# Optimization experiments

Hardware: AMD Instinct MI355X
Metric: run time of the kernel (lower is better)

## Reference

```python
import jax, jax.numpy as jnp
import numpy as np

INPUT_DIM, LATENT_DIM, HIDDEN_DIM, BATCH = 1024, 128, 1024, 32768


def setup_inputs() -> dict:
    key = jax.random.key(0)
    ks = jax.random.split(key, 12)
    s = 0.02
    x = (jax.random.uniform(ks[0], (BATCH, INPUT_DIM)) < 0.5).astype(jnp.float32)  # binary data
    eps = jax.random.normal(ks[1], (BATCH, LATENT_DIM), dtype=jnp.float32)
    return {
        "x": x,
        "eps": eps,
        "We1": jax.random.normal(ks[2], (INPUT_DIM, HIDDEN_DIM)) * s,
        "be1": jnp.zeros((HIDDEN_DIM,), jnp.float32),
        "Wmu": jax.random.normal(ks[3], (HIDDEN_DIM, LATENT_DIM)) * s,
        "bmu": jnp.zeros((LATENT_DIM,), jnp.float32),
        "Wls": jax.random.normal(ks[4], (HIDDEN_DIM, LATENT_DIM)) * s,
        "bls": jnp.zeros((LATENT_DIM,), jnp.float32),
        "Wd1": jax.random.normal(ks[5], (LATENT_DIM, HIDDEN_DIM)) * s,
        "bd1": jnp.zeros((HIDDEN_DIM,), jnp.float32),
        "Wd2": jax.random.normal(ks[6], (HIDDEN_DIM, INPUT_DIM)) * s,
        "bd2": jnp.zeros((INPUT_DIM,), jnp.float32),
    }


def reference(x, eps, We1, be1, Wmu, bmu, Wls, bls, Wd1, bd1, Wd2, bd2):
    # Encoder: one hidden ReLU layer, mu / logsigma heads
    h = jax.nn.relu(x @ We1 + be1)                      # [B, H]
    mu = h @ Wmu + bmu                                  # [B, L]
    logsigma = h @ Wls + bls                            # [B, L]
    # Reparameterization: z = sigma * eps + mu (vectorized diag(exp(logsigma)) @ eps)
    z = mu + jnp.exp(logsigma) * eps                    # [B, L]
    # Decoder: one hidden ReLU layer, sigmoid Bernoulli params
    hd = jax.nn.relu(z @ Wd1 + bd1)                     # [B, H]
    theta = jax.nn.sigmoid(hd @ Wd2 + bd2)              # [B, D]
    # Bernoulli log-likelihood: sum_j log(theta^x * (1-theta)^(1-x))
    log_px = jnp.sum(x * jnp.log(theta) + (1.0 - x) * jnp.log1p(-theta), axis=-1)  # [B]
    # KL(q||N(0,I)) = 0.5 * sum(sigma^2 + mu^2 - log(sigma^2) - 1)
    kl = 0.5 * jnp.sum(jnp.exp(2.0 * logsigma) + mu * mu - 2.0 * logsigma - 1.0, axis=-1)  # [B]
    return log_px - kl                                  # elbo_mc [B]
```

## Files before the change

kernel.cpp:

```cpp
#include <hip/hip_runtime.h>
#include <cstdint>
#include <cstddef>


typedef __bf16 bf16x8 __attribute__((ext_vector_type(8)));
typedef float f32x4 __attribute__((ext_vector_type(4)));

__device__ __forceinline__ unsigned short f32_to_bf16(float f) {
  unsigned int u = __float_as_uint(f);
  u += 0x7fffu + ((u >> 16) & 1u);
  return (unsigned short)(u >> 16);
}

__global__ void cast_bf16_k(const float* __restrict__ in,
                            unsigned short* __restrict__ out, int n4) {
  int stride = gridDim.x * blockDim.x;
  for (int i = blockIdx.x * blockDim.x + threadIdx.x; i < n4; i += stride) {
    float4 v = reinterpret_cast<const float4*>(in)[i];
    ushort4 o = make_ushort4(f32_to_bf16(v.x), f32_to_bf16(v.y),
                             f32_to_bf16(v.z), f32_to_bf16(v.w));
    reinterpret_cast<ushort4*>(out)[i] = o;
  }
}

struct TransJob { const float* in; unsigned short* out; int K, N, blkEnd; };

__global__ void transpose_all_k(TransJob j0, TransJob j1, TransJob j2,
                                TransJob j3, TransJob j4) {
  __shared__ float tile[32][33];
  int bid = blockIdx.x;
  TransJob j; int base;
  if (bid < j0.blkEnd)      { j = j0; base = 0; }
  else if (bid < j1.blkEnd) { j = j1; base = j0.blkEnd; }
  else if (bid < j2.blkEnd) { j = j2; base = j1.blkEnd; }
  else if (bid < j3.blkEnd) { j = j3; base = j2.blkEnd; }
  else                      { j = j4; base = j3.blkEnd; }
  int local = bid - base;
  int gxN = j.N >> 5;
  int n0 = (local % gxN) * 32, k0 = (local / gxN) * 32;
  int tx = threadIdx.x, ty = threadIdx.y;
#pragma unroll
  for (int r = 0; r < 32; r += 8)
    tile[ty + r][tx] = j.in[(size_t)(k0 + ty + r) * j.N + n0 + tx];
  __syncthreads();
#pragma unroll
  for (int r = 0; r < 32; r += 8)
    j.out[(size_t)(n0 + ty + r) * j.K + k0 + tx] = f32_to_bf16(tile[tx][ty + r]);
}

__device__ __forceinline__ void gl_lds16(const unsigned short* g, unsigned short* l) {
  __builtin_amdgcn_global_load_lds(
      (__attribute__((address_space(1))) void*)g,
      (__attribute__((address_space(3))) void*)l, 16, 0, 0);
}

template <int EPI>
__global__ __launch_bounds__(256) void gemm_bt(
    const unsigned short* __restrict__ A, const unsigned short* __restrict__ BT,
    int gx, int N, int K,
    const float* __restrict__ bias0,
    unsigned short* __restrict__ outb, float* __restrict__ outf,
    const unsigned short* __restrict__ xbf) {
  __shared__ __align__(16) unsigned short As[128 * 64];
  __shared__ __align__(16) unsigned short Bs[128 * 64];

  const int tid = threadIdx.x;
  const int lane = tid & 63;
  const int wave = tid >> 6;
  const int wr = wave >> 1, wc = wave & 1;
  const int bid = blockIdx.x;
  const int xcd = bid & 7;
  const int t8 = bid >> 3;
  const int m0 = (xcd + 8 * (t8 / gx)) * 128;
  const int n0 = (t8 % gx) * 128;
  const int lm = lane & 15, lq = lane >> 4;

  const unsigned short* agp[4];
  const unsigned short* bgp[4];
#pragma unroll
  for (int r = 0; r < 4; ++r) {
    int c = tid + 256 * r;
    int row = c >> 3, q = (c & 7) ^ (row & 7);
    agp[r] = A + (size_t)(m0 + row) * K + q * 8;
    bgp[r] = BT + (size_t)(n0 + row) * K + q * 8;
  }
  const int sw = lm & 7;

  f32x4 acc[4][4] = {};

  for (int kt = 0; kt < K; kt += 64) {
#pragma unroll
    for (int r = 0; r < 4; ++r) {
      gl_lds16(agp[r] + kt, As + (tid + 256 * r) * 8);
      gl_lds16(bgp[r] + kt, Bs + (tid + 256 * r) * 8);
    }
    __syncthreads();

#pragma unroll
    for (int s = 0; s < 2; ++s) {
      const int so = ((s << 2) | lq) ^ sw;
      bf16x8 af[4], bfr[4];
#pragma unroll
      for (int i = 0; i < 4; ++i)
        af[i] = *reinterpret_cast<const bf16x8*>(As + (wr * 64 + i * 16 + lm) * 64 + so * 8);
#pragma unroll
      for (int j = 0; j < 4; ++j)
        bfr[j] = *reinterpret_cast<const bf16x8*>(Bs + (wc * 64 + j * 16 + lm) * 64 + so * 8);
#pragma unroll
      for (int i = 0; i < 4; ++i)
#pragma unroll
        for (int j = 0; j < 4; ++j)
          acc[i][j] = __builtin_amdgcn_mfma_f32_16x16x32_bf16(af[i], bfr[j], acc[i][j], 0, 0, 0);
    }
    __syncthreads();
  }

  if (EPI == 0) {
#pragma unroll
    for (int i = 0; i < 4; ++i)
#pragma unroll
      for (int j = 0; j < 4; ++j) {
        int col = n0 + wc * 64 + j * 16 + lm;
        float bias = bias0[col];
#pragma unroll
        for (int r = 0; r < 4; ++r) {
          int row = m0 + wr * 64 + i * 16 + lq * 4 + r;
          float v = acc[i][j][r] + bias;
          v = fmaxf(v, 0.f);
          outb[(size_t)row * N + col] = f32_to_bf16(v);
        }
      }
  } else {
#pragma unroll
    for (int i = 0; i < 4; ++i) {
      float rs[4] = {0.f, 0.f, 0.f, 0.f};
#pragma unroll
      for (int j = 0; j < 4; ++j) {
        int col = n0 + wc * 64 + j * 16 + lm;
        float bias = bias0[col];
#pragma unroll
        for (int r = 0; r < 4; ++r) {
          int row = m0 + wr * 64 + i * 16 + lq * 4 + r;
          float l = acc[i][j][r] + bias;
          unsigned short xb = xbf[(size_t)row * N + col];
          float t = xb ? -l : l;
          float sp = fmaxf(t, 0.f) + __logf(1.f + __expf(-fabsf(t)));
          rs[r] -= sp;
        }
      }
#pragma unroll
      for (int off = 1; off < 16; off <<= 1)
#pragma unroll
        for (int r = 0; r < 4; ++r) rs[r] += __shfl_xor(rs[r], off, 64);
      if (lm == 0) {
#pragma unroll
        for (int r = 0; r < 4; ++r)
          atomicAdd(&outf[m0 + wr * 64 + i * 16 + lq * 4 + r], rs[r]);
      }
    }
  }
}

__global__ __launch_bounds__(256, 1) void gemm2_zkl(
    const unsigned short* __restrict__ A,
    const unsigned short* __restrict__ BT,
    int K,
    const float* __restrict__ bmu, const float* __restrict__ bls,
    const float* __restrict__ eps,
    unsigned short* __restrict__ z,
    float* __restrict__ out) {
  __shared__ __align__(16) unsigned short As[128 * 64];
  __shared__ __align__(16) unsigned short Bs[256 * 64];

  const int tid = threadIdx.x;
  const int lane = tid & 63;
  const int wave = tid >> 6;
  const int m0 = blockIdx.x * 128;
  const int lm = lane & 15, lq = lane >> 4;

  const unsigned short* agp[4];
  const unsigned short* bgp[8];
#pragma unroll
  for (int r = 0; r < 4; ++r) {
    int c = tid + 256 * r;
    int row = c >> 3, q = (c & 7) ^ (row & 7);
    agp[r] = A + (size_t)(m0 + row) * K + q * 8;
  }
#pragma unroll
  for (int r = 0; r < 8; ++r) {
    int c = tid + 256 * r;
    int row = c >> 3, q = (c & 7) ^ (row & 7);
    bgp[r] = BT + (size_t)row * K + q * 8;
  }
  const int sw = lm & 7;

  f32x4 acc[2][16] = {};

  for (int kt = 0; kt < K; kt += 64) {
#pragma unroll
    for (int r = 0; r < 4; ++r) gl_lds16(agp[r] + kt, As + (tid + 256 * r) * 8);
#pragma unroll
    for (int r = 0; r < 8; ++r) gl_lds16(bgp[r] + kt, Bs + (tid + 256 * r) * 8);
    __syncthreads();

#pragma unroll
    for (int s = 0; s < 2; ++s) {
      const int so = ((s << 2) | lq) ^ sw;
      bf16x8 af[2];
#pragma unroll
      for (int i = 0; i < 2; ++i)
        af[i] = *reinterpret_cast<const bf16x8*>(As + (wave * 32 + i * 16 + lm) * 64 + so * 8);
#pragma unroll
      for (int j = 0; j < 16; ++j) {
        bf16x8 b = *reinterpret_cast<const bf16x8*>(Bs + (j * 16 + lm) * 64 + so * 8);
        acc[0][j] = __builtin_amdgcn_mfma_f32_16x16x32_bf16(af[0], b, acc[0][j], 0, 0, 0);
        acc[1][j] = __builtin_amdgcn_mfma_f32_16x16x32_bf16(af[1], b, acc[1][j], 0, 0, 0);
      }
    }
    __syncthreads();
  }

#pragma unroll
  for (int i = 0; i < 2; ++i) {
    float kl[4] = {0.f, 0.f, 0.f, 0.f};
#pragma unroll
    for (int j = 0; j < 8; ++j) {
      int dim = j * 16 + lm;
      float bm = bmu[dim], bl = bls[dim];
#pragma unroll
      for (int r = 0; r < 4; ++r) {
        int row = m0 + wave * 32 + i * 16 + lq * 4 + r;
        float mu = acc[i][j][r] + bm;
        float ls = acc[i][j + 8][r] + bl;
        float e = eps[(size_t)row * 128 + dim];
        z[(size_t)row * 128 + dim] = f32_to_bf16(fmaf(__expf(ls), e, mu));
        kl[r] += 0.5f * (__expf(2.f * ls) + mu * mu - 2.f * ls - 1.f);
      }
    }
#pragma unroll
    for (int off = 1; off < 16; off <<= 1)
#pragma unroll
      for (int r = 0; r < 4; ++r) kl[r] += __shfl_xor(kl[r], off, 64);
    if (lm == 0) {
#pragma unroll
      for (int r = 0; r < 4; ++r)
        out[m0 + wave * 32 + i * 16 + lq * 4 + r] = -kl[r];
    }
  }
}

extern "C" void kernel_launch(void* const* d_in, const int* in_sizes, int n_in,
                              void* d_out, int out_size, void* d_ws, size_t ws_size,
                              hipStream_t stream) {
  const float* x   = (const float*)d_in[0];
  const float* eps = (const float*)d_in[1];
  const float* We1 = (const float*)d_in[2];
  const float* be1 = (const float*)d_in[3];
  const float* Wmu = (const float*)d_in[4];
  const float* bmu = (const float*)d_in[5];
  const float* Wls = (const float*)d_in[6];
  const float* bls = (const float*)d_in[7];
  const float* Wd1 = (const float*)d_in[8];
  const float* bd1 = (const float*)d_in[9];
  const float* Wd2 = (const float*)d_in[10];
  const float* bd2 = (const float*)d_in[11];
  float* out = (float*)d_out;

  const int B = 32768, D = 1024, H = 1024, L = 128;

  char* ws = (char*)d_ws;
  size_t off = 0;
  auto alloc = [&](size_t bytes) {
    void* p = ws + off;
    off += (bytes + 255) & ~(size_t)255;
    return p;
  };
  unsigned short* xbf  = (unsigned short*)alloc((size_t)B * D * 2);
  unsigned short* w1t  = (unsigned short*)alloc((size_t)H * D * 2);
  unsigned short* w2t  = (unsigned short*)alloc((size_t)256 * H * 2);
  unsigned short* wd1t = (unsigned short*)alloc((size_t)H * L * 2);
  unsigned short* wd2t = (unsigned short*)alloc((size_t)D * H * 2);
  unsigned short* h    = (unsigned short*)alloc((size_t)B * H * 2);
  unsigned short* z    = (unsigned short*)alloc((size_t)B * L * 2);
  unsigned short* hd   = h;

  cast_bf16_k<<<2048, 256, 0, stream>>>(x, xbf, B * D / 4);

  TransJob j0{We1, w1t, D, H, 1024};
  TransJob j1{Wmu, w2t, H, L, 1152};
  TransJob j2{Wls, w2t + 128 * H, H, L, 1280};
  TransJob j3{Wd1, wd1t, L, H, 1408};
  TransJob j4{Wd2, wd2t, H, D, 2432};
  transpose_all_k<<<2432, dim3(32, 8), 0, stream>>>(j0, j1, j2, j3, j4);

  gemm_bt<0><<<8 * 256, 256, 0, stream>>>(
      xbf, w1t, 8, H, D, be1, h, nullptr, nullptr);
  gemm2_zkl<<<B / 128, 256, 0, stream>>>(h, w2t, H, bmu, bls, eps, z, out);
  gemm_bt<0><<<8 * 256, 256, 0, stream>>>(
      z, wd1t, 8, H, L, bd1, hd, nullptr, nullptr);
  gemm_bt<2><<<8 * 256, 256, 0, stream>>>(
      hd, wd2t, 8, D, H, bd2, nullptr, out, xbf);

  (void)in_sizes; (void)n_in; (void)out_size; (void)ws_size;
}
```

Baseline: 470.4 us.

## Replace 128x128 GEMM with 256x256 double-buffered 8-wave pipelined kernel

Replaces the 128x128-tile, 4-wave GEMM used for the encoder hidden layer and both decoder layers with a 256x256-tile, 8-wave kernel. The new kernel double-buffers LDS and splits each K step into four quadrant sub-phases, interleaving async global-to-LDS loads with MFMA work under explicit barriers, waitcnts and setprio. The aim is to raise arithmetic intensity and hide load latency behind compute. The risks are much larger LDS use (128KB per block), higher register pressure from 32 accumulators per lane, and only 512 blocks, which may leave the grid short of waves.

New measurement: 435.5 us. 1.08x faster.

```diff
diff --git a/kernel.cpp b/kernel.cpp
--- a/kernel.cpp
+++ b/kernel.cpp
@@ -55,84 +55,166 @@
 }
 
 template <int EPI>
-__global__ __launch_bounds__(256) void gemm_bt(
+__global__ __launch_bounds__(512, 2) void gemm256(
     const unsigned short* __restrict__ A, const unsigned short* __restrict__ BT,
     int gx, int N, int K,
     const float* __restrict__ bias0,
     unsigned short* __restrict__ outb, float* __restrict__ outf,
     const unsigned short* __restrict__ xbf) {
-  __shared__ __align__(16) unsigned short As[128 * 64];
-  __shared__ __align__(16) unsigned short Bs[128 * 64];
+  __shared__ __align__(16) unsigned short lds[2][2][256 * 64];
 
   const int tid = threadIdx.x;
   const int lane = tid & 63;
   const int wave = tid >> 6;
-  const int wr = wave >> 1, wc = wave & 1;
+  const int wr = wave >> 2;
+  const int wc = wave & 3;
+  const int lm = lane & 15, lq = lane >> 4;
+  const int sw = lm & 7;
+
   const int bid = blockIdx.x;
   const int xcd = bid & 7;
   const int t8 = bid >> 3;
-  const int m0 = (xcd + 8 * (t8 / gx)) * 128;
-  const int n0 = (t8 % gx) * 128;
-  const int lm = lane & 15, lq = lane >> 4;
-
-  const unsigned short* agp[4];
-  const unsigned short* bgp[4];
-#pragma unroll
-  for (int r = 0; r < 4; ++r) {
-    int c = tid + 256 * r;
-    int row = c >> 3, q = (c & 7) ^ (row & 7);
-    agp[r] = A + (size_t)(m0 + row) * K + q * 8;
-    bgp[r] = BT + (size_t)(n0 + row) * K + q * 8;
-  }
-  const int sw = lm & 7;
-
-  f32x4 acc[4][4] = {};
-
-  for (int kt = 0; kt < K; kt += 64) {
-#pragma unroll
-    for (int r = 0; r < 4; ++r) {
-      gl_lds16(agp[r] + kt, As + (tid + 256 * r) * 8);
-      gl_lds16(bgp[r] + kt, Bs + (tid + 256 * r) * 8);
-    }
-    __syncthreads();
-
-#pragma unroll
-    for (int s = 0; s < 2; ++s) {
-      const int so = ((s << 2) | lq) ^ sw;
-      bf16x8 af[4], bfr[4];
+  const int m0 = (xcd + 8 * (t8 / gx)) * 256;
+  const int n0 = (t8 % gx) * 256;
+  const int NT = K >> 6;
+
+  const unsigned short* gpA[2];
+  const unsigned short* gpB[2];
+  int loA[2], loB[2];
+#pragma unroll
+  for (int r = 0; r < 2; ++r) {
+    int c = tid + 512 * r, rl = c >> 3, q8 = c & 7;
+    int rowA = (rl & 63) + ((rl >> 6) << 7);
+    int rowB = (rl & 31) + ((rl >> 5) << 6);
+    gpA[r] = A + (size_t)(m0 + rowA) * K + (q8 ^ (rowA & 7)) * 8;
+    gpB[r] = BT + (size_t)(n0 + rowB) * K + (q8 ^ (rowB & 7)) * 8;
+    loA[r] = rowA * 64 + q8 * 8;
+    loB[r] = rowB * 64 + q8 * 8;
+  }
+
+  auto stage = [&](int kind, int buf, int kt) {
+#pragma unroll
+    for (int r = 0; r < 2; ++r) {
+      if (kind == 0)      gl_lds16(gpA[r] + kt * 64,          &lds[buf][0][loA[r]]);
+      else if (kind == 3) gl_lds16(gpA[r] + 64 * K + kt * 64, &lds[buf][0][loA[r] + 64 * 64]);
+      else if (kind == 1) gl_lds16(gpB[r] + kt * 64,          &lds[buf][1][loB[r]]);
+      else                gl_lds16(gpB[r] + 32 * K + kt * 64, &lds[buf][1][loB[r] + 32 * 64]);
+    }
+  };
+
+  stage(0, 0, 0); stage(1, 0, 0); stage(2, 0, 0); stage(3, 0, 0);
+  stage(0, 1, 1); stage(1, 1, 1); stage(2, 1, 1);
+  asm volatile("s_waitcnt vmcnt(6)" ::: "memory");
+  __builtin_amdgcn_s_barrier();
+
+  f32x4 acc[8][4] = {};
+
+  const int aRow = (wr * 128 + lm) * 64;
+  const int bRow = (wc * 64 + lm) * 64;
+  const int c0 = ((0 | lq) ^ sw) * 8;
+  const int c1 = ((4 | lq) ^ sw) * 8;
+
+  for (int t = 0; t < NT; ++t) {
+    const int b = t & 1;
+    const unsigned short* Ab = &lds[b][0][0];
+    const unsigned short* Bb = &lds[b][1][0];
+    bf16x8 af[4][2], bf1[2][2], bf2[2][2];
+
+#pragma unroll
+    for (int i = 0; i < 4; ++i) {
+      af[i][0] = *reinterpret_cast<const bf16x8*>(Ab + aRow + i * 16 * 64 + c0);
+      af[i][1] = *reinterpret_cast<const bf16x8*>(Ab + aRow + i * 16 * 64 + c1);
+    }
+#pragma unroll
+    for (int j = 0; j < 2; ++j) {
+      bf1[j][0] = *reinterpret_cast<const bf16x8*>(Bb + bRow + j * 16 * 64 + c0);
+      bf1[j][1] = *reinterpret_cast<const bf16x8*>(Bb + bRow + j * 16 * 64 + c1);
+    }
+    if (t + 1 < NT) stage(3, (t + 1) & 1, t + 1);
+    __builtin_amdgcn_s_barrier();
+    asm volatile("s_waitcnt lgkmcnt(0)" ::: "memory");
+    __builtin_amdgcn_s_setprio(1);
+#pragma unroll
+    for (int s = 0; s < 2; ++s)
 #pragma unroll
       for (int i = 0; i < 4; ++i)
-        af[i] = *reinterpret_cast<const bf16x8*>(As + (wr * 64 + i * 16 + lm) * 64 + so * 8);
-#pragma unroll
-      for (int j = 0; j < 4; ++j)
-        bfr[j] = *reinterpret_cast<const bf16x8*>(Bs + (wc * 64 + j * 16 + lm) * 64 + so * 8);
+#pragma unroll
+        for (int j = 0; j < 2; ++j)
+          acc[i][j] = __builtin_amdgcn_mfma_f32_16x16x32_bf16(af[i][s], bf1[j][s], acc[i][j], 0, 0, 0);
+    __builtin_amdgcn_s_setprio(0);
+    __builtin_amdgcn_s_barrier();
+
+#pragma unroll
+    for (int j = 0; j < 2; ++j) {
+      bf2[j][0] = *reinterpret_cast<const bf16x8*>(Bb + bRow + (j + 2) * 16 * 64 + c0);
+      bf2[j][1] = *reinterpret_cast<const bf16x8*>(Bb + bRow + (j + 2) * 16 * 64 + c1);
+    }
+    if (t + 2 < NT) stage(0, b, t + 2);
+    __builtin_amdgcn_s_barrier();
+    asm volatile("s_waitcnt lgkmcnt(0)" ::: "memory");
+    __builtin_amdgcn_s_setprio(1);
+#pragma unroll
+    for (int s = 0; s < 2; ++s)
 #pragma unroll
       for (int i = 0; i < 4; ++i)
 #pragma unroll
-        for (int j = 0; j < 4; ++j)
-          acc[i][j] = __builtin_amdgcn_mfma_f32_16x16x32_bf16(af[i], bfr[j], acc[i][j], 0, 0, 0);
-    }
-    __syncthreads();
+        for (int j = 0; j < 2; ++j)
+          acc[i][j + 2] = __builtin_amdgcn_mfma_f32_16x16x32_bf16(af[i][s], bf2[j][s], acc[i][j + 2], 0, 0, 0);
+    __builtin_amdgcn_s_setprio(0);
+    __builtin_amdgcn_s_barrier();
+
+#pragma unroll
+    for (int i = 0; i < 4; ++i) {
+      af[i][0] = *reinterpret_cast<const bf16x8*>(Ab + aRow + (64 + i * 16) * 64 + c0);
+      af[i][1] = *reinterpret_cast<const bf16x8*>(Ab + aRow + (64 + i * 16) * 64 + c1);
+    }
+    if (t + 2 < NT) stage(1, b, t + 2);
+    __builtin_amdgcn_s_barrier();
+    asm volatile("s_waitcnt lgkmcnt(0)" ::: "memory");
+    __builtin_amdgcn_s_setprio(1);
+#pragma unroll
+    for (int s = 0; s < 2; ++s)
+#pragma unroll
+      for (int i = 0; i < 4; ++i)
+#pragma unroll
+        for (int j = 0; j < 2; ++j)
+          acc[i + 4][j] = __builtin_amdgcn_mfma_f32_16x16x32_bf16(af[i][s], bf1[j][s], acc[i + 4][j], 0, 0, 0);
+    __builtin_amdgcn_s_setprio(0);
+    __builtin_amdgcn_s_barrier();
+
+    if (t + 2 < NT) stage(2, b, t + 2);
+    __builtin_amdgcn_s_barrier();
+    __builtin_amdgcn_s_setprio(1);
+#pragma unroll
+    for (int s = 0; s < 2; ++s)
+#pragma unroll
+      for (int i = 0; i < 4; ++i)
+#pragma unroll
+        for (int j = 0; j < 2; ++j)
+          acc[i + 4][j + 2] = __builtin_amdgcn_mfma_f32_16x16x32_bf16(af[i][s], bf2[j][s], acc[i + 4][j + 2], 0, 0, 0);
+    __builtin_amdgcn_s_setprio(0);
+    if (t + 2 < NT)      { asm volatile("s_waitcnt vmcnt(6)" ::: "memory"); }
+    else if (t + 1 < NT) { asm volatile("s_waitcnt vmcnt(0)" ::: "memory"); }
+    __builtin_amdgcn_s_barrier();
   }
 
   if (EPI == 0) {
 #pragma unroll
-    for (int i = 0; i < 4; ++i)
+    for (int i = 0; i < 8; ++i)
 #pragma unroll
       for (int j = 0; j < 4; ++j) {
         int col = n0 + wc * 64 + j * 16 + lm;
         float bias = bias0[col];
 #pragma unroll
         for (int r = 0; r < 4; ++r) {
-          int row = m0 + wr * 64 + i * 16 + lq * 4 + r;
+          int row = m0 + wr * 128 + i * 16 + lq * 4 + r;
           float v = acc[i][j][r] + bias;
-          v = fmaxf(v, 0.f);
-          outb[(size_t)row * N + col] = f32_to_bf16(v);
+          outb[(size_t)row * N + col] = f32_to_bf16(fmaxf(v, 0.f));
         }
       }
   } else {
 #pragma unroll
-    for (int i = 0; i < 4; ++i) {
+    for (int i = 0; i < 8; ++i) {
       float rs[4] = {0.f, 0.f, 0.f, 0.f};
 #pragma unroll
       for (int j = 0; j < 4; ++j) {
@@ -140,11 +222,11 @@
         float bias = bias0[col];
 #pragma unroll
         for (int r = 0; r < 4; ++r) {
-          int row = m0 + wr * 64 + i * 16 + lq * 4 + r;
+          int row = m0 + wr * 128 + i * 16 + lq * 4 + r;
           float l = acc[i][j][r] + bias;
           unsigned short xb = xbf[(size_t)row * N + col];
-          float t = xb ? -l : l;
-          float sp = fmaxf(t, 0.f) + __logf(1.f + __expf(-fabsf(t)));
+          float tt = xb ? -l : l;
+          float sp = fmaxf(tt, 0.f) + __logf(1.f + __expf(-fabsf(tt)));
           rs[r] -= sp;
         }
       }
@@ -155,7 +237,7 @@
       if (lm == 0) {
 #pragma unroll
         for (int r = 0; r < 4; ++r)
-          atomicAdd(&outf[m0 + wr * 64 + i * 16 + lq * 4 + r], rs[r]);
+          atomicAdd(&outf[m0 + wr * 128 + i * 16 + lq * 4 + r], rs[r]);
       }
     }
   }
@@ -293,13 +375,13 @@
   TransJob j4{Wd2, wd2t, H, D, 2432};
   transpose_all_k<<<2432, dim3(32, 8), 0, stream>>>(j0, j1, j2, j3, j4);
 
-  gemm_bt<0><<<8 * 256, 256, 0, stream>>>(
-      xbf, w1t, 8, H, D, be1, h, nullptr, nullptr);
+  gemm256<0><<<512, 512, 0, stream>>>(
+      xbf, w1t, 4, H, D, be1, h, nullptr, nullptr);
   gemm2_zkl<<<B / 128, 256, 0, stream>>>(h, w2t, H, bmu, bls, eps, z, out);
-  gemm_bt<0><<<8 * 256, 256, 0, stream>>>(
-      z, wd1t, 8, H, L, bd1, hd, nullptr, nullptr);
-  gemm_bt<2><<<8 * 256, 256, 0, stream>>>(
-      hd, wd2t, 8, D, H, bd2, nullptr, out, xbf);
+  gemm256<0><<<512, 512, 0, stream>>>(
+      z, wd1t, 4, H, L, bd1, hd, nullptr, nullptr);
+  gemm256<2><<<512, 512, 0, stream>>>(
+      hd, wd2t, 4, D, H, bd2, nullptr, out, xbf);
 
   (void)in_sizes; (void)n_in; (void)out_size; (void)ws_size;
 }
```

## Double-buffer GEMM LDS tiles with K=32 steps and prefetch next tile

Applied to the files above, without the earlier changes.

Rewrites the shared 128x128 GEMM kernel to use two LDS buffers of 128x32 bf16 tiles. The next K slice is loaded via global_load_lds while MFMAs run on the current one, so each step needs one barrier instead of two. It also adds launch_bounds occupancy 4, a new XOR swizzle for the 32-wide rows, and s_setprio around the MFMA block. Total LDS stays the same, but each K step does half as much MFMA work, which adds per-iteration sync overhead.

After: 450.0 us. 4.3% less time.

```diff
diff --git a/kernel.cpp b/kernel.cpp
--- a/kernel.cpp
+++ b/kernel.cpp
@@ -55,64 +55,79 @@
 }
 
 template <int EPI>
-__global__ __launch_bounds__(256) void gemm_bt(
+__global__ __launch_bounds__(256, 4) void gemm128(
     const unsigned short* __restrict__ A, const unsigned short* __restrict__ BT,
     int gx, int N, int K,
     const float* __restrict__ bias0,
     unsigned short* __restrict__ outb, float* __restrict__ outf,
     const unsigned short* __restrict__ xbf) {
-  __shared__ __align__(16) unsigned short As[128 * 64];
-  __shared__ __align__(16) unsigned short Bs[128 * 64];
+  __shared__ __align__(16) unsigned short As[2][128 * 32];
+  __shared__ __align__(16) unsigned short Bs[2][128 * 32];
 
   const int tid = threadIdx.x;
   const int lane = tid & 63;
   const int wave = tid >> 6;
   const int wr = wave >> 1, wc = wave & 1;
+  const int lm = lane & 15, lq = lane >> 4;
   const int bid = blockIdx.x;
   const int xcd = bid & 7;
   const int t8 = bid >> 3;
   const int m0 = (xcd + 8 * (t8 / gx)) * 128;
   const int n0 = (t8 % gx) * 128;
-  const int lm = lane & 15, lq = lane >> 4;
-
-  const unsigned short* agp[4];
-  const unsigned short* bgp[4];
-#pragma unroll
-  for (int r = 0; r < 4; ++r) {
-    int c = tid + 256 * r;
-    int row = c >> 3, q = (c & 7) ^ (row & 7);
-    agp[r] = A + (size_t)(m0 + row) * K + q * 8;
-    bgp[r] = BT + (size_t)(n0 + row) * K + q * 8;
-  }
-  const int sw = lm & 7;
+  const int NT = K >> 5;
+
+  const unsigned short* agp[2];
+  const unsigned short* bgp[2];
+#pragma unroll
+  for (int r = 0; r < 2; ++r) {
+    int c = tid + 256 * r, row = c >> 2, q = c & 3;
+    int qg = q ^ ((row >> 1) & 3);
+    agp[r] = A + (size_t)(m0 + row) * K + qg * 8;
+    bgp[r] = BT + (size_t)(n0 + row) * K + qg * 8;
+  }
+
+  const int sw2 = (lm >> 1) & 3;
+  const int aOff = (wr * 64 + lm) * 32 + (lq ^ sw2) * 8;
+  const int bOff = (wc * 64 + lm) * 32 + (lq ^ sw2) * 8;
 
   f32x4 acc[4][4] = {};
 
-  for (int kt = 0; kt < K; kt += 64) {
-#pragma unroll
-    for (int r = 0; r < 4; ++r) {
-      gl_lds16(agp[r] + kt, As + (tid + 256 * r) * 8);
-      gl_lds16(bgp[r] + kt, Bs + (tid + 256 * r) * 8);
-    }
-    __syncthreads();
-
-#pragma unroll
-    for (int s = 0; s < 2; ++s) {
-      const int so = ((s << 2) | lq) ^ sw;
-      bf16x8 af[4], bfr[4];
-#pragma unroll
-      for (int i = 0; i < 4; ++i)
-        af[i] = *reinterpret_cast<const bf16x8*>(As + (wr * 64 + i * 16 + lm) * 64 + so * 8);
+#pragma unroll
+  for (int r = 0; r < 2; ++r) gl_lds16(agp[r], &As[0][(tid + 256 * r) * 8]);
+#pragma unroll
+  for (int r = 0; r < 2; ++r) gl_lds16(bgp[r], &Bs[0][(tid + 256 * r) * 8]);
+  asm volatile("s_waitcnt vmcnt(0)" ::: "memory");
+  __builtin_amdgcn_s_barrier();
+
+  for (int t = 0; t < NT; ++t) {
+    const int cur = t & 1;
+    if (t + 1 < NT) {
+      const int nk = (t + 1) << 5;
+#pragma unroll
+      for (int r = 0; r < 2; ++r)
+        gl_lds16(agp[r] + nk, &As[cur ^ 1][(tid + 256 * r) * 8]);
+#pragma unroll
+      for (int r = 0; r < 2; ++r)
+        gl_lds16(bgp[r] + nk, &Bs[cur ^ 1][(tid + 256 * r) * 8]);
+    }
+    bf16x8 af[4], bfr[4];
+#pragma unroll
+    for (int i = 0; i < 4; ++i)
+      af[i] = *reinterpret_cast<const bf16x8*>(&As[cur][aOff + i * 512]);
+#pragma unroll
+    for (int j = 0; j < 4; ++j)
+      bfr[j] = *reinterpret_cast<const bf16x8*>(&Bs[cur][bOff + j * 512]);
+    asm volatile("s_waitcnt lgkmcnt(0)" ::: "memory");
+    __builtin_amdgcn_sched_barrier(0);
+    __builtin_amdgcn_s_setprio(1);
+#pragma unroll
+    for (int i = 0; i < 4; ++i)
 #pragma unroll
       for (int j = 0; j < 4; ++j)
-        bfr[j] = *reinterpret_cast<const bf16x8*>(Bs + (wc * 64 + j * 16 + lm) * 64 + so * 8);
-#pragma unroll
-      for (int i = 0; i < 4; ++i)
-#pragma unroll
-        for (int j = 0; j < 4; ++j)
-          acc[i][j] = __builtin_amdgcn_mfma_f32_16x16x32_bf16(af[i], bfr[j], acc[i][j], 0, 0, 0);
-    }
-    __syncthreads();
+        acc[i][j] = __builtin_amdgcn_mfma_f32_16x16x32_bf16(af[i], bfr[j], acc[i][j], 0, 0, 0);
+    __builtin_amdgcn_s_setprio(0);
+    if (t + 1 < NT) { asm volatile("s_waitcnt vmcnt(0)" ::: "memory"); }
+    __builtin_amdgcn_s_barrier();
   }
 
   if (EPI == 0) {
@@ -126,8 +141,7 @@
         for (int r = 0; r < 4; ++r) {
           int row = m0 + wr * 64 + i * 16 + lq * 4 + r;
           float v = acc[i][j][r] + bias;
-          v = fmaxf(v, 0.f);
-          outb[(size_t)row * N + col] = f32_to_bf16(v);
+          outb[(size_t)row * N + col] = f32_to_bf16(fmaxf(v, 0.f));
         }
       }
   } else {
@@ -143,8 +157,8 @@
           int row = m0 + wr * 64 + i * 16 + lq * 4 + r;
           float l = acc[i][j][r] + bias;
           unsigned short xb = xbf[(size_t)row * N + col];
-          float t = xb ? -l : l;
-          float sp = fmaxf(t, 0.f) + __logf(1.f + __expf(-fabsf(t)));
+          float tt = xb ? -l : l;
+          float sp = fmaxf(tt, 0.f) + __logf(1.f + __expf(-fabsf(tt)));
           rs[r] -= sp;
         }
       }
@@ -293,12 +307,12 @@
   TransJob j4{Wd2, wd2t, H, D, 2432};
   transpose_all_k<<<2432, dim3(32, 8), 0, stream>>>(j0, j1, j2, j3, j4);
 
-  gemm_bt<0><<<8 * 256, 256, 0, stream>>>(
+  gemm128<0><<<8 * 256, 256, 0, stream>>>(
       xbf, w1t, 8, H, D, be1, h, nullptr, nullptr);
   gemm2_zkl<<<B / 128, 256, 0, stream>>>(h, w2t, H, bmu, bls, eps, z, out);
-  gemm_bt<0><<<8 * 256, 256, 0, stream>>>(
+  gemm128<0><<<8 * 256, 256, 0, stream>>>(
       z, wd1t, 8, H, L, bd1, hd, nullptr, nullptr);
-  gemm_bt<2><<<8 * 256, 256, 0, stream>>>(
+  gemm128<2><<<8 * 256, 256, 0, stream>>>(
       hd, wd2t, 8, D, H, bd2, nullptr, out, xbf);
 
   (void)in_sizes; (void)n_in; (void)out_size; (void)ws_size;
```

## Fuse latent and decoder layer-1 GEMMs, double-buffer tiles, bit-pack x mask

Applied to the files above, without the earlier changes.

The mu/logsigma GEMM is merged with the first decoder GEMM. The reparameterised z stays in LDS as a swizzled tile and is multiplied by Wd1 tiles streamed into the reused staging buffers, so the z buffer and one kernel launch go away. The generic GEMM now double-buffers its A/B LDS tiles so the next k-tile loads while the current one computes, and it requests two blocks per CU. The cast kernel also packs x into a 1-bit mask, so the log-likelihood epilogue reads bits instead of bf16 values. In exchange this uses much more LDS per block (64 KB in the GEMM, 128 KB in the fused kernel), which can limit occupancy, and correctness depends on global-to-LDS loads completing before the barriers.

After: 453.0 us. 1.04x faster.

```diff
diff --git a/kernel.cpp b/kernel.cpp
--- a/kernel.cpp
+++ b/kernel.cpp
@@ -13,13 +13,21 @@
 }
 
 __global__ void cast_bf16_k(const float* __restrict__ in,
-                            unsigned short* __restrict__ out, int n4) {
+                            unsigned short* __restrict__ out,
+                            unsigned short* __restrict__ xbit, int n4) {
   int stride = gridDim.x * blockDim.x;
   for (int i = blockIdx.x * blockDim.x + threadIdx.x; i < n4; i += stride) {
     float4 v = reinterpret_cast<const float4*>(in)[i];
     ushort4 o = make_ushort4(f32_to_bf16(v.x), f32_to_bf16(v.y),
                              f32_to_bf16(v.z), f32_to_bf16(v.w));
     reinterpret_cast<ushort4*>(out)[i] = o;
+    unsigned int nib = (v.x != 0.f ? 1u : 0u) | (v.y != 0.f ? 2u : 0u) |
+                       (v.z != 0.f ? 4u : 0u) | (v.w != 0.f ? 8u : 0u);
+    unsigned int n1 = __shfl_down(nib, 1, 64);
+    unsigned int n2 = __shfl_down(nib, 2, 64);
+    unsigned int n3 = __shfl_down(nib, 3, 64);
+    if ((threadIdx.x & 3) == 0)
+      xbit[i >> 2] = (unsigned short)(nib | (n1 << 4) | (n2 << 8) | (n3 << 12));
   }
 }
 
@@ -54,26 +62,28 @@
       (__attribute__((address_space(3))) void*)l, 16, 0, 0);
 }
 
-template <int EPI>
-__global__ __launch_bounds__(256) void gemm_bt(
+template <int EPI, int TAG>
+__global__ __launch_bounds__(256, 2) void gemm128(
     const unsigned short* __restrict__ A, const unsigned short* __restrict__ BT,
     int gx, int N, int K,
     const float* __restrict__ bias0,
     unsigned short* __restrict__ outb, float* __restrict__ outf,
-    const unsigned short* __restrict__ xbf) {
-  __shared__ __align__(16) unsigned short As[128 * 64];
-  __shared__ __align__(16) unsigned short Bs[128 * 64];
+    const unsigned short* __restrict__ xbit) {
+  __shared__ __align__(16) unsigned short As[2][128 * 64];
+  __shared__ __align__(16) unsigned short Bs[2][128 * 64];
 
   const int tid = threadIdx.x;
   const int lane = tid & 63;
   const int wave = tid >> 6;
   const int wr = wave >> 1, wc = wave & 1;
+  const int lm = lane & 15, lq = lane >> 4;
+  const int sw = lm & 7;
   const int bid = blockIdx.x;
   const int xcd = bid & 7;
   const int t8 = bid >> 3;
   const int m0 = (xcd + 8 * (t8 / gx)) * 128;
   const int n0 = (t8 % gx) * 128;
-  const int lm = lane & 15, lq = lane >> 4;
+  const int NT = K >> 6;
 
   const unsigned short* agp[4];
   const unsigned short* bgp[4];
@@ -84,17 +94,23 @@
     agp[r] = A + (size_t)(m0 + row) * K + q * 8;
     bgp[r] = BT + (size_t)(n0 + row) * K + q * 8;
   }
-  const int sw = lm & 7;
+
+  auto stage = [&](int buf, int kt) {
+#pragma unroll
+    for (int r = 0; r < 4; ++r) {
+      gl_lds16(agp[r] + kt, &As[buf][(tid + 256 * r) * 8]);
+      gl_lds16(bgp[r] + kt, &Bs[buf][(tid + 256 * r) * 8]);
+    }
+  };
 
   f32x4 acc[4][4] = {};
 
-  for (int kt = 0; kt < K; kt += 64) {
-#pragma unroll
-    for (int r = 0; r < 4; ++r) {
-      gl_lds16(agp[r] + kt, As + (tid + 256 * r) * 8);
-      gl_lds16(bgp[r] + kt, Bs + (tid + 256 * r) * 8);
-    }
-    __syncthreads();
+  stage(0, 0);
+  __syncthreads();
+
+  for (int t = 0; t < NT; ++t) {
+    const int cur = t & 1;
+    if (t + 1 < NT) stage(cur ^ 1, (t + 1) * 64);
 
 #pragma unroll
     for (int s = 0; s < 2; ++s) {
@@ -102,10 +118,10 @@
       bf16x8 af[4], bfr[4];
 #pragma unroll
       for (int i = 0; i < 4; ++i)
-        af[i] = *reinterpret_cast<const bf16x8*>(As + (wr * 64 + i * 16 + lm) * 64 + so * 8);
+        af[i] = *reinterpret_cast<const bf16x8*>(&As[cur][(wr * 64 + i * 16 + lm) * 64 + so * 8]);
 #pragma unroll
       for (int j = 0; j < 4; ++j)
-        bfr[j] = *reinterpret_cast<const bf16x8*>(Bs + (wc * 64 + j * 16 + lm) * 64 + so * 8);
+        bfr[j] = *reinterpret_cast<const bf16x8*>(&Bs[cur][(wc * 64 + j * 16 + lm) * 64 + so * 8]);
 #pragma unroll
       for (int i = 0; i < 4; ++i)
 #pragma unroll
@@ -126,11 +142,11 @@
         for (int r = 0; r < 4; ++r) {
           int row = m0 + wr * 64 + i * 16 + lq * 4 + r;
           float v = acc[i][j][r] + bias;
-          v = fmaxf(v, 0.f);
-          outb[(size_t)row * N + col] = f32_to_bf16(v);
+          outb[(size_t)row * N + col] = f32_to_bf16(fmaxf(v, 0.f));
         }
       }
   } else {
+    const int wpr = N >> 4;
 #pragma unroll
     for (int i = 0; i < 4; ++i) {
       float rs[4] = {0.f, 0.f, 0.f, 0.f};
@@ -138,13 +154,14 @@
       for (int j = 0; j < 4; ++j) {
         int col = n0 + wc * 64 + j * 16 + lm;
         float bias = bias0[col];
+        int w16 = (col >> 4);
 #pragma unroll
         for (int r = 0; r < 4; ++r) {
           int row = m0 + wr * 64 + i * 16 + lq * 4 + r;
           float l = acc[i][j][r] + bias;
-          unsigned short xb = xbf[(size_t)row * N + col];
-          float t = xb ? -l : l;
-          float sp = fmaxf(t, 0.f) + __logf(1.f + __expf(-fabsf(t)));
+          unsigned short mask = xbit[(size_t)row * wpr + w16];
+          float tt = ((mask >> lm) & 1) ? -l : l;
+          float sp = fmaxf(tt, 0.f) + __logf(1.f + __expf(-fabsf(tt)));
           rs[r] -= sp;
         }
       }
@@ -161,22 +178,30 @@
   }
 }
 
-__global__ __launch_bounds__(256, 1) void gemm2_zkl(
-    const unsigned short* __restrict__ A,
+__global__ __launch_bounds__(256, 1) void latent_fused(
+    const unsigned short* A,
     const unsigned short* __restrict__ BT,
-    int K,
+    const unsigned short* __restrict__ WD1,
     const float* __restrict__ bmu, const float* __restrict__ bls,
+    const float* __restrict__ bd1,
     const float* __restrict__ eps,
-    unsigned short* __restrict__ z,
+    unsigned short* hd,
     float* __restrict__ out) {
-  __shared__ __align__(16) unsigned short As[128 * 64];
-  __shared__ __align__(16) unsigned short Bs[256 * 64];
-
+  __shared__ __align__(16) unsigned short smem[65536];
+  unsigned short* As0 = smem;
+  unsigned short* As1 = smem + 8192;
+  unsigned short* Bs0 = smem + 16384;
+  unsigned short* Bs1 = smem + 32768;
+  unsigned short* zs  = smem + 49152;
+  unsigned short* Bs2 = smem;
+
+  const int K = 1024;
   const int tid = threadIdx.x;
   const int lane = tid & 63;
   const int wave = tid >> 6;
   const int m0 = blockIdx.x * 128;
   const int lm = lane & 15, lq = lane >> 4;
+  const int sw = lm & 7;
 
   const unsigned short* agp[4];
   const unsigned short* bgp[8];
@@ -192,33 +217,53 @@
     int row = c >> 3, q = (c & 7) ^ (row & 7);
     bgp[r] = BT + (size_t)row * K + q * 8;
   }
-  const int sw = lm & 7;
+
+  auto stage1 = [&](int buf, int kt) {
+    unsigned short* Ad = buf ? As1 : As0;
+    unsigned short* Bd = buf ? Bs1 : Bs0;
+#pragma unroll
+    for (int r = 0; r < 4; ++r) gl_lds16(agp[r] + kt, Ad + (tid + 256 * r) * 8);
+#pragma unroll
+    for (int r = 0; r < 8; ++r) gl_lds16(bgp[r] + kt, Bd + (tid + 256 * r) * 8);
+  };
 
   f32x4 acc[2][16] = {};
 
-  for (int kt = 0; kt < K; kt += 64) {
-#pragma unroll
-    for (int r = 0; r < 4; ++r) gl_lds16(agp[r] + kt, As + (tid + 256 * r) * 8);
-#pragma unroll
-    for (int r = 0; r < 8; ++r) gl_lds16(bgp[r] + kt, Bs + (tid + 256 * r) * 8);
-    __syncthreads();
-
+  stage1(0, 0);
+  __syncthreads();
+
+  for (int t = 0; t < 16; ++t) {
+    const int cur = t & 1;
+    if (t + 1 < 16) stage1(cur ^ 1, (t + 1) * 64);
+    const unsigned short* Ab = cur ? As1 : As0;
+    const unsigned short* Bb = cur ? Bs1 : Bs0;
 #pragma unroll
     for (int s = 0; s < 2; ++s) {
       const int so = ((s << 2) | lq) ^ sw;
       bf16x8 af[2];
 #pragma unroll
       for (int i = 0; i < 2; ++i)
-        af[i] = *reinterpret_cast<const bf16x8*>(As + (wave * 32 + i * 16 + lm) * 64 + so * 8);
+        af[i] = *reinterpret_cast<const bf16x8*>(Ab + (wave * 32 + i * 16 + lm) * 64 + so * 8);
 #pragma unroll
       for (int j = 0; j < 16; ++j) {
-        bf16x8 b = *reinterpret_cast<const bf16x8*>(Bs + (j * 16 + lm) * 64 + so * 8);
+        bf16x8 b = *reinterpret_cast<const bf16x8*>(Bb + (j * 16 + lm) * 64 + so * 8);
         acc[0][j] = __builtin_amdgcn_mfma_f32_16x16x32_bf16(af[0], b, acc[0][j], 0, 0, 0);
         acc[1][j] = __builtin_amdgcn_mfma_f32_16x16x32_bf16(af[1], b, acc[1][j], 0, 0, 0);
       }
     }
     __syncthreads();
   }
+
+  auto stage2 = [&](int nt) {
+#pragma unroll
+    for (int ri = 0; ri < 16; ++ri) {
+      int c = tid + 256 * ri;
+      int row = c >> 4, slot = c & 15;
+      int gc = slot ^ (row & 7);
+      gl_lds16(WD1 + (size_t)(nt * 256 + row) * 128 + gc * 8, Bs2 + c * 8);
+    }
+  };
+  stage2(0);
 
 #pragma unroll
   for (int i = 0; i < 2; ++i) {
@@ -229,11 +274,14 @@
       float bm = bmu[dim], bl = bls[dim];
 #pragma unroll
       for (int r = 0; r < 4; ++r) {
-        int row = m0 + wave * 32 + i * 16 + lq * 4 + r;
+        int rowl = wave * 32 + i * 16 + lq * 4 + r;
         float mu = acc[i][j][r] + bm;
         float ls = acc[i][j + 8][r] + bl;
-        float e = eps[(size_t)row * 128 + dim];
-        z[(size_t)row * 128 + dim] = f32_to_bf16(fmaf(__expf(ls), e, mu));
+        float e = eps[(size_t)(m0 + rowl) * 128 + dim];
+        float zv = fmaf(__expf(ls), e, mu);
+        int chunk = (dim >> 3);
+        int slot = chunk ^ (rowl & 7);
+        zs[rowl * 128 + slot * 8 + (lm & 7)] = f32_to_bf16(zv);
         kl[r] += 0.5f * (__expf(2.f * ls) + mu * mu - 2.f * ls - 1.f);
       }
     }
@@ -246,6 +294,39 @@
       for (int r = 0; r < 4; ++r)
         out[m0 + wave * 32 + i * 16 + lq * 4 + r] = -kl[r];
     }
+  }
+
+  for (int nt = 0; nt < 4; ++nt) {
+    asm volatile("s_waitcnt vmcnt(0)" ::: "memory");
+    __syncthreads();
+    f32x4 acc2[2][16] = {};
+#pragma unroll
+    for (int ks = 0; ks < 4; ++ks) {
+      const int cks = (ks * 4 + lq) ^ (lm & 7);
+      bf16x8 a0 = *reinterpret_cast<const bf16x8*>(zs + (wave * 32 + lm) * 128 + cks * 8);
+      bf16x8 a1 = *reinterpret_cast<const bf16x8*>(zs + (wave * 32 + 16 + lm) * 128 + cks * 8);
+#pragma unroll
+      for (int j = 0; j < 16; ++j) {
+        bf16x8 b = *reinterpret_cast<const bf16x8*>(Bs2 + (j * 16 + lm) * 128 + cks * 8);
+        acc2[0][j] = __builtin_amdgcn_mfma_f32_16x16x32_bf16(a0, b, acc2[0][j], 0, 0, 0);
+        acc2[1][j] = __builtin_amdgcn_mfma_f32_16x16x32_bf16(a1, b, acc2[1][j], 0, 0, 0);
+      }
+    }
+    __syncthreads();
+    if (nt + 1 < 4) stage2(nt + 1);
+#pragma unroll
+    for (int i = 0; i < 2; ++i)
+#pragma unroll
+      for (int j = 0; j < 16; ++j) {
+        int col = nt * 256 + j * 16 + lm;
+        float bias = bd1[col];
+#pragma unroll
+        for (int r = 0; r < 4; ++r) {
+          int row = m0 + wave * 32 + i * 16 + lq * 4 + r;
+          float v = acc2[i][j][r] + bias;
+          hd[(size_t)row * 1024 + col] = f32_to_bf16(fmaxf(v, 0.f));
+        }
+      }
   }
 }
 
@@ -276,15 +357,15 @@
     return p;
   };
   unsigned short* xbf  = (unsigned short*)alloc((size_t)B * D * 2);
+  unsigned short* xbit = (unsigned short*)alloc((size_t)B * D / 8);
   unsigned short* w1t  = (unsigned short*)alloc((size_t)H * D * 2);
   unsigned short* w2t  = (unsigned short*)alloc((size_t)256 * H * 2);
   unsigned short* wd1t = (unsigned short*)alloc((size_t)H * L * 2);
   unsigned short* wd2t = (unsigned short*)alloc((size_t)D * H * 2);
   unsigned short* h    = (unsigned short*)alloc((size_t)B * H * 2);
-  unsigned short* z    = (unsigned short*)alloc((size_t)B * L * 2);
   unsigned short* hd   = h;
 
-  cast_bf16_k<<<2048, 256, 0, stream>>>(x, xbf, B * D / 4);
+  cast_bf16_k<<<2048, 256, 0, stream>>>(x, xbf, xbit, B * D / 4);
 
   TransJob j0{We1, w1t, D, H, 1024};
   TransJob j1{Wmu, w2t, H, L, 1152};
@@ -293,13 +374,12 @@
   TransJob j4{Wd2, wd2t, H, D, 2432};
   transpose_all_k<<<2432, dim3(32, 8), 0, stream>>>(j0, j1, j2, j3, j4);
 
-  gemm_bt<0><<<8 * 256, 256, 0, stream>>>(
+  gemm128<0, 1><<<8 * 256, 256, 0, stream>>>(
       xbf, w1t, 8, H, D, be1, h, nullptr, nullptr);
-  gemm2_zkl<<<B / 128, 256, 0, stream>>>(h, w2t, H, bmu, bls, eps, z, out);
-  gemm_bt<0><<<8 * 256, 256, 0, stream>>>(
-      z, wd1t, 8, H, L, bd1, hd, nullptr, nullptr);
-  gemm_bt<2><<<8 * 256, 256, 0, stream>>>(
-      hd, wd2t, 8, D, H, bd2, nullptr, out, xbf);
+  latent_fused<<<B / 128, 256, 0, stream>>>(
+      h, w2t, wd1t, bmu, bls, bd1, eps, hd, out);
+  gemm128<2, 4><<<8 * 256, 256, 0, stream>>>(
+      hd, wd2t, 8, D, H, bd2, nullptr, out, xbit);
 
   (void)in_sizes; (void)n_in; (void)out_size; (void)ws_size;
 }
```
